# Kernel tuning notes

Hardware: AMD Instinct MI355X
Metric: run time of the kernel (lower is better)

## Reference

```python
import jax, jax.numpy as jnp
import numpy as np

N_NODES = 100000
N_EDGES = 1600000
D = 128
D_FF = 2 * D
BN_EPS = 1e-5


def setup_inputs() -> dict:
    key = jax.random.key(0)
    ks = jax.random.split(key, 16)
    s = lambda k, shp, fan: jax.random.normal(k, shp, jnp.float32) / np.float32(np.sqrt(fan))
    return {
        "x": jax.random.normal(ks[0], (N_NODES, D), jnp.float32),
        "edge_attr": jax.random.normal(ks[1], (N_EDGES, D), jnp.float32),
        "w1g": s(ks[2], (D, D), D),
        "b1g": jnp.zeros((D,), jnp.float32),
        "w2g": s(ks[3], (D, D), D),
        "b2g": jnp.zeros((D,), jnp.float32),
        "bn1_g": jax.random.uniform(ks[4], (D,), jnp.float32, 0.5, 1.5),
        "bn1_b": 0.1 * jax.random.normal(ks[5], (D,), jnp.float32),
        "ff_w1": s(ks[6], (D, D_FF), D),
        "ff_b1": jnp.zeros((D_FF,), jnp.float32),
        "ff_w2": s(ks[7], (D_FF, D), D_FF),
        "ff_b2": jnp.zeros((D,), jnp.float32),
        "bn2_g": jax.random.uniform(ks[8], (D,), jnp.float32, 0.5, 1.5),
        "bn2_b": 0.1 * jax.random.normal(ks[9], (D,), jnp.float32),
        "edge_index": jax.random.randint(ks[10], (2, N_EDGES), 0, N_NODES, jnp.int64 if jax.config.jax_enable_x64 else jnp.int32),
    }


def _batchnorm(h, gamma, beta):
    # training-mode BatchNorm1d: per-batch (node-axis) stats, biased variance
    mean = h.mean(axis=0)
    var = ((h - mean) ** 2).mean(axis=0)
    return gamma * (h - mean) * jax.lax.rsqrt(var + BN_EPS) + beta


def reference(x, edge_attr, w1g, b1g, w2g, b2g, bn1_g, bn1_b,
              ff_w1, ff_b1, ff_w2, ff_b2, bn2_g, bn2_b, edge_index):
    src, dst = edge_index[0], edge_index[1]
    # GINEConv message: relu(x_j + e_ij), scatter-sum into target nodes
    msg = jax.nn.relu(x[src] + edge_attr)                      # [E, D]
    agg = jax.ops.segment_sum(msg, dst, num_segments=N_NODES)  # [N, D]
    h = x + agg                                                # (1+eps)*x with eps=0
    # gin_nn: Linear -> ReLU -> Linear
    h = jax.nn.relu(h @ w1g + b1g) @ w2g + b2g
    h = jax.nn.relu(h)                                         # post-conv relu; dropout=identity (eval)
    h = x + h                                                  # residual
    h = _batchnorm(h, bn1_g, bn1_b)                            # norm1_local
    ff = jax.nn.relu(h @ ff_w1 + ff_b1) @ ff_w2 + ff_b2        # FFN block (dropouts identity)
    h = h + ff
    h = _batchnorm(h, bn2_g, bn2_b)                            # norm2
    return h
```

## Files before the change

### kernel.cpp

```cpp
#include <hip/hip_runtime.h>
#include <hip/hip_bf16.h>

#define NN 100000
#define NE 1600000
#define DD 128
#define DFF 256
#define BN_EPS 1e-5f
#define NND ((size_t)NN * DD)
#define NTILE 6250
#define CAP 64

typedef __attribute__((ext_vector_type(8))) short short8;
typedef __attribute__((ext_vector_type(4))) float f32x4;
typedef __attribute__((ext_vector_type(4))) unsigned short us4;

static __device__ __forceinline__ unsigned short f2bf(float f) {
  union { float f; unsigned u; } v; v.f = f;
  unsigned r = v.u + 0x7fffu + ((v.u >> 16) & 1u);
  return (unsigned short)(r >> 16);
}
static __device__ __forceinline__ float bf2f(unsigned short h) {
  union { unsigned u; float f; } v; v.u = ((unsigned)h) << 16;
  return v.f;
}

__global__ __launch_bounds__(256) void k_prep(const float* __restrict__ x,
    unsigned short* __restrict__ xbf,
    const float* __restrict__ w1g, const float* __restrict__ w2g,
    const float* __restrict__ ffw1, const float* __restrict__ ffw2,
    unsigned short* __restrict__ w1t, unsigned short* __restrict__ w2t,
    unsigned short* __restrict__ fw1t, unsigned short* __restrict__ fw2t) {
  int b = blockIdx.x;
  if (b < 6250) {
    size_t base = ((size_t)b * 256u + threadIdx.x) * 8;
    const f32x4* xp = reinterpret_cast<const f32x4*>(x + base);
    f32x4 a0 = xp[0], a1 = xp[1];
    short8 o;
#pragma unroll
    for (int j = 0; j < 4; ++j) o[j] = (short)f2bf(a0[j]);
#pragma unroll
    for (int j = 0; j < 4; ++j) o[4 + j] = (short)f2bf(a1[j]);
    *reinterpret_cast<short8*>(xbf + base) = o;
  } else {
    int i = (b - 6250) * 256 + threadIdx.x;
    if (i < 16384) { int c = i & 127, k = i >> 7; w1t[c * 128 + k] = f2bf(w1g[k * 128 + c]); }
    else if (i < 32768) { i -= 16384; int c = i & 127, k = i >> 7; w2t[c * 128 + k] = f2bf(w2g[k * 128 + c]); }
    else if (i < 65536) { i -= 32768; int c = i & 255, k = i >> 8; fw1t[c * 128 + k] = f2bf(ffw1[k * 256 + c]); }
    else if (i < 98304) { i -= 65536; int c = i & 127, k = i >> 7; fw2t[c * 256 + k] = f2bf(ffw2[k * 128 + c]); }
  }
}

__global__ __launch_bounds__(256) void k_scatter(const int* __restrict__ ei,
                                                 int* __restrict__ cnt,
                                                 int2* __restrict__ el2) {
  int e = blockIdx.x * 256 + threadIdx.x;
  if (e >= NE) return;
  int s = ei[e], d = ei[NE + e];
  int p = atomicAdd(&cnt[d], 1);
  if (p < CAP) el2[d * CAP + p] = make_int2(e, s);
}

__global__ __launch_bounds__(256) void k_gather(
    const unsigned short* __restrict__ xbf, const float* __restrict__ ea,
    const int* __restrict__ cnt, const int2* __restrict__ el2,
    unsigned short* __restrict__ h0) {
  int n = blockIdx.x * 8 + (threadIdx.x >> 5);
  int q = threadIdx.x & 31;
  int deg = cnt[n];
  deg = deg > CAP ? CAP : deg;
  int beg = n * CAP;
  int end = beg + deg;
  f32x4 acc = (f32x4){0.f, 0.f, 0.f, 0.f};
  int2 E0 = make_int2(0, 0), E1 = E0, E2 = E0, E3 = E0;
  int i = beg;
  if (i     < end) E0 = el2[i];
  if (i + 1 < end) E1 = el2[i + 1];
  if (i + 2 < end) E2 = el2[i + 2];
  if (i + 3 < end) E3 = el2[i + 3];
  for (; i + 4 <= end; i += 4) {
    f32x4 ev0 = *(reinterpret_cast<const f32x4*>(ea + (size_t)E0.x * DD) + q);
    us4  xv0 = *reinterpret_cast<const us4*>(xbf + (size_t)E0.y * DD + q * 4);
    f32x4 ev1 = *(reinterpret_cast<const f32x4*>(ea + (size_t)E1.x * DD) + q);
    us4  xv1 = *reinterpret_cast<const us4*>(xbf + (size_t)E1.y * DD + q * 4);
    f32x4 ev2 = *(reinterpret_cast<const f32x4*>(ea + (size_t)E2.x * DD) + q);
    us4  xv2 = *reinterpret_cast<const us4*>(xbf + (size_t)E2.y * DD + q * 4);
    f32x4 ev3 = *(reinterpret_cast<const f32x4*>(ea + (size_t)E3.x * DD) + q);
    us4  xv3 = *reinterpret_cast<const us4*>(xbf + (size_t)E3.y * DD + q * 4);
    int2 N0 = E0, N1 = E1, N2 = E2, N3 = E3;
    if (i + 4 < end) N0 = el2[i + 4];
    if (i + 5 < end) N1 = el2[i + 5];
    if (i + 6 < end) N2 = el2[i + 6];
    if (i + 7 < end) N3 = el2[i + 7];
#pragma unroll
    for (int c = 0; c < 4; ++c) {
      float m0 = bf2f((unsigned short)xv0[c]) + ev0[c];
      acc[c] += (m0 > 0.f) ? m0 : 0.f;
      float m1 = bf2f((unsigned short)xv1[c]) + ev1[c];
      acc[c] += (m1 > 0.f) ? m1 : 0.f;
      float m2 = bf2f((unsigned short)xv2[c]) + ev2[c];
      acc[c] += (m2 > 0.f) ? m2 : 0.f;
      float m3 = bf2f((unsigned short)xv3[c]) + ev3[c];
      acc[c] += (m3 > 0.f) ? m3 : 0.f;
    }
    E0 = N0; E1 = N1; E2 = N2; E3 = N3;
  }
  if (i < end) {
    f32x4 ev = *(reinterpret_cast<const f32x4*>(ea + (size_t)E0.x * DD) + q);
    us4  xv = *reinterpret_cast<const us4*>(xbf + (size_t)E0.y * DD + q * 4);
#pragma unroll
    for (int c = 0; c < 4; ++c) {
      float m = bf2f((unsigned short)xv[c]) + ev[c];
      acc[c] += (m > 0.f) ? m : 0.f;
    }
  }
  if (i + 1 < end) {
    f32x4 ev = *(reinterpret_cast<const f32x4*>(ea + (size_t)E1.x * DD) + q);
    us4  xv = *reinterpret_cast<const us4*>(xbf + (size_t)E1.y * DD + q * 4);
#pragma unroll
    for (int c = 0; c < 4; ++c) {
      float m = bf2f((unsigned short)xv[c]) + ev[c];
      acc[c] += (m > 0.f) ? m : 0.f;
    }
  }
  if (i + 2 < end) {
    f32x4 ev = *(reinterpret_cast<const f32x4*>(ea + (size_t)E2.x * DD) + q);
    us4  xv = *reinterpret_cast<const us4*>(xbf + (size_t)E2.y * DD + q * 4);
#pragma unroll
    for (int c = 0; c < 4; ++c) {
      float m = bf2f((unsigned short)xv[c]) + ev[c];
      acc[c] += (m > 0.f) ? m : 0.f;
    }
  }
  us4 xs = *reinterpret_cast<const us4*>(xbf + (size_t)n * DD + q * 4);
  union { unsigned short us[4]; unsigned long long u; } pk;
#pragma unroll
  for (int c = 0; c < 4; ++c) pk.us[c] = f2bf(bf2f((unsigned short)xs[c]) + acc[c]);
  *reinterpret_cast<unsigned long long*>(h0 + (size_t)n * DD + q * 4) = pk.u;
}

#define TR1 136
__global__ __launch_bounds__(256) void k_mlp1(const unsigned short* __restrict__ A,
    const unsigned short* __restrict__ W1T, const float* __restrict__ b1,
    const unsigned short* __restrict__ W2T, const float* __restrict__ b2,
    const unsigned short* __restrict__ xbf, float* __restrict__ O,
    float* __restrict__ stats) {
  __shared__ unsigned short tr[4][16 * TR1];
  __shared__ float lds_s[128], lds_q[128];
  if (threadIdx.x < 128) { lds_s[threadIdx.x] = 0.f; lds_q[threadIdx.x] = 0.f; }
  int lane = threadIdx.x & 63, w = threadIdx.x >> 6;
  int tile = blockIdx.x * 4 + w;
  int l15 = lane & 15, g = lane >> 4;
  int row0 = tile * 16;
  __syncthreads();
  if (tile < NTILE) {
    f32x4 acc[8];
#pragma unroll
    for (int ct = 0; ct < 8; ++ct) {
      float b = b1[ct * 16 + l15];
      acc[ct] = (f32x4){b, b, b, b};
    }
    short8 a[4];
#pragma unroll
    for (int kt = 0; kt < 4; ++kt)
      a[kt] = *reinterpret_cast<const short8*>(A + (size_t)(row0 + l15) * DD + kt * 32 + g * 8);
#pragma unroll
    for (int kt = 0; kt < 4; ++kt) {
      int k0 = kt * 32 + g * 8;
#pragma unroll
      for (int ct = 0; ct < 8; ++ct) {
        int c = ct * 16 + l15;
        short8 b = *reinterpret_cast<const short8*>(W1T + (size_t)c * DD + k0);
        acc[ct] = __builtin_amdgcn_mfma_f32_16x16x32_bf16(a[kt], b, acc[ct], 0, 0, 0);
      }
    }
#pragma unroll
    for (int ct = 0; ct < 8; ++ct)
#pragma unroll
      for (int r = 0; r < 4; ++r) {
        float v = acc[ct][r];
        v = v > 0.f ? v : 0.f;
        tr[w][(g * 4 + r) * TR1 + ct * 16 + l15] = f2bf(v);
      }
  }
  __syncthreads();
  if (tile < NTILE) {
    short8 a2[4];
#pragma unroll
    for (int kt = 0; kt < 4; ++kt)
      a2[kt] = *reinterpret_cast<const short8*>(&tr[w][l15 * TR1 + kt * 32 + g * 8]);
    f32x4 acc2[8];
#pragma unroll
    for (int ct = 0; ct < 8; ++ct) {
      float b = b2[ct * 16 + l15];
      acc2[ct] = (f32x4){b, b, b, b};
    }
#pragma unroll
    for (int kt = 0; kt < 4; ++kt) {
      int k0 = kt * 32 + g * 8;
#pragma unroll
      for (int ct = 0; ct < 8; ++ct) {
        int c = ct * 16 + l15;
        short8 b = *reinterpret_cast<const short8*>(W2T + (size_t)c * DD + k0);
        acc2[ct] = __builtin_amdgcn_mfma_f32_16x16x32_bf16(a2[kt], b, acc2[ct], 0, 0, 0);
      }
    }
#pragma unroll
    for (int ct = 0; ct < 8; ++ct) {
      int c = ct * 16 + l15;
      float s = 0.f, q = 0.f;
#pragma unroll
      for (int r = 0; r < 4; ++r) {
        int row = row0 + g * 4 + r;
        float v = acc2[ct][r];
        v = v > 0.f ? v : 0.f;
        v += bf2f(xbf[(size_t)row * DD + c]);
        O[(size_t)row * DD + c] = v;
        s += v; q += v * v;
      }
      s += __shfl_xor(s, 16); s += __shfl_xor(s, 32);
      q += __shfl_xor(q, 16); q += __shfl_xor(q, 32);
      if (g == 0) { atomicAdd(&lds_s[c], s); atomicAdd(&lds_q[c], q); }
    }
  }
  __syncthreads();
  if (threadIdx.x < 128) {
    atomicAdd(&stats[threadIdx.x], lds_s[threadIdx.x]);
    atomicAdd(&stats[128 + threadIdx.x], lds_q[threadIdx.x]);
  }
}

#define TR2 264
__global__ __launch_bounds__(256) void k_mlp2(const float* __restrict__ H,
    const float* __restrict__ stats, const float* __restrict__ bn1g,
    const float* __restrict__ bn1b, const unsigned short* __restrict__ FW1T,
    const float* __restrict__ fb1, const unsigned short* __restrict__ FW2T,
    const float* __restrict__ fb2, float* __restrict__ O, float* __restrict__ stats2) {
  __shared__ unsigned short tr[4][16 * TR2];
  __shared__ float lds_s[128], lds_q[128], ldspar[256];
  int t = threadIdx.x;
  if (t < 128) {
    lds_s[t] = 0.f; lds_q[t] = 0.f;
    float mean = stats[t] * (1.f / NN);
    float var = stats[128 + t] * (1.f / NN) - mean * mean;
    float sc = bn1g[t] * rsqrtf(var + BN_EPS);
    ldspar[t] = sc;
    ldspar[128 + t] = bn1b[t] - mean * sc;
  }
  int lane = t & 63, w = t >> 6;
  int tile = blockIdx.x * 4 + w;
  int l15 = lane & 15, g = lane >> 4;
  int row0 = tile * 16;
  __syncthreads();
  if (tile < NTILE) {
    const float* arow = H + (size_t)(row0 + l15) * DD;
    short8 a1[4];
#pragma unroll
    for (int kt = 0; kt < 4; ++kt) {
      int k0 = kt * 32 + g * 8;
      f32x4 u0 = *reinterpret_cast<const f32x4*>(arow + k0);
      f32x4 u1 = *reinterpret_cast<const f32x4*>(arow + k0 + 4);
      short8 af;
#pragma unroll
      for (int j = 0; j < 4; ++j)
        af[j] = (short)f2bf(ldspar[k0 + j] * u0[j] + ldspar[128 + k0 + j]);
#pragma unroll
      for (int j = 0; j < 4; ++j)
        af[4 + j] = (short)f2bf(ldspar[k0 + 4 + j] * u1[j] + ldspar[128 + k0 + 4 + j]);
      a1[kt] = af;
    }
    f32x4 acc1[16];
#pragma unroll
    for (int ct = 0; ct < 16; ++ct) {
      float b = fb1[ct * 16 + l15];
      acc1[ct] = (f32x4){b, b, b, b};
    }
#pragma unroll
    for (int kt = 0; kt < 4; ++kt) {
      int k0 = kt * 32 + g * 8;
#pragma unroll
      for (int ct = 0; ct < 16; ++ct) {
        int c = ct * 16 + l15;
        short8 b = *reinterpret_cast<const short8*>(FW1T + (size_t)c * DD + k0);
        acc1[ct] = __builtin_amdgcn_mfma_f32_16x16x32_bf16(a1[kt], b, acc1[ct], 0, 0, 0);
      }
    }
#pragma unroll
    for (int ct = 0; ct < 16; ++ct)
#pragma unroll
      for (int r = 0; r < 4; ++r) {
        float v = acc1[ct][r];
        v = v > 0.f ? v : 0.f;
        tr[w][(g * 4 + r) * TR2 + ct * 16 + l15] = f2bf(v);
      }
  }
  __syncthreads();
  if (tile < NTILE) {
    short8 a2[8];
#pragma unroll
    for (int kt = 0; kt < 8; ++kt)
      a2[kt] = *reinterpret_cast<const short8*>(&tr[w][l15 * TR2 + kt * 32 + g * 8]);
    f32x4 acc2[8];
#pragma unroll
    for (int ct = 0; ct < 8; ++ct) {
      float b = fb2[ct * 16 + l15];
      acc2[ct] = (f32x4){b, b, b, b};
    }
#pragma unroll 2
    for (int kt = 0; kt < 8; ++kt) {
      int k0 = kt * 32 + g * 8;
#pragma unroll
      for (int ct = 0; ct < 8; ++ct) {
        int c = ct * 16 + l15;
        short8 b = *reinterpret_cast<const short8*>(FW2T + (size_t)c * DFF + k0);
        acc2[ct] = __builtin_amdgcn_mfma_f32_16x16x32_bf16(a2[kt], b, acc2[ct], 0, 0, 0);
      }
    }
#pragma unroll
    for (int ct = 0; ct < 8; ++ct) {
      int c = ct * 16 + l15;
      float sc = ldspar[c], sh = ldspar[128 + c];
      float s = 0.f, q = 0.f;
#pragma unroll
      for (int r = 0; r < 4; ++r) {
        int row = row0 + g * 4 + r;
        float h1v = sc * O[(size_t)row * DD + c] + sh;
        float v = acc2[ct][r] + h1v;
        O[(size_t)row * DD + c] = v;
        s += v; q += v * v;
      }
      s += __shfl_xor(s, 16); s += __shfl_xor(s, 32);
      q += __shfl_xor(q, 16); q += __shfl_xor(q, 32);
      if (g == 0) { atomicAdd(&lds_s[c], s); atomicAdd(&lds_q[c], q); }
    }
  }
  __syncthreads();
  if (t < 128) {
    atomicAdd(&stats2[t], lds_s[t]);
    atomicAdd(&stats2[128 + t], lds_q[t]);
  }
}

__global__ __launch_bounds__(256) void k_bnfinal(float* __restrict__ h,
    const float* __restrict__ st, const float* __restrict__ gm,
    const float* __restrict__ bt) {
  size_t base = ((size_t)blockIdx.x * 256u + threadIdx.x) * 4;
  int c0 = (int)(base & 127);
  f32x4 v = *reinterpret_cast<f32x4*>(h + base);
#pragma unroll
  for (int j = 0; j < 4; ++j) {
    int c = c0 + j;
    float mean = st[c] * (1.f / NN);
    float var = st[128 + c] * (1.f / NN) - mean * mean;
    float sc = gm[c] * rsqrtf(var + BN_EPS);
    float sh = bt[c] - mean * sc;
    v[j] = sc * v[j] + sh;
  }
  *reinterpret_cast<f32x4*>(h + base) = v;
}

extern "C" void kernel_launch(void* const* d_in, const int* in_sizes, int n_in,
                              void* d_out, int out_size, void* d_ws, size_t ws_size,
                              hipStream_t stream) {
  const float* x    = (const float*)d_in[0];
  const float* ea   = (const float*)d_in[1];
  const float* w1g  = (const float*)d_in[2];
  const float* b1g  = (const float*)d_in[3];
  const float* w2g  = (const float*)d_in[4];
  const float* b2g  = (const float*)d_in[5];
  const float* bn1g = (const float*)d_in[6];
  const float* bn1b = (const float*)d_in[7];
  const float* ffw1 = (const float*)d_in[8];
  const float* ffb1 = (const float*)d_in[9];
  const float* ffw2 = (const float*)d_in[10];
  const float* ffb2 = (const float*)d_in[11];
  const float* bn2g = (const float*)d_in[12];
  const float* bn2b = (const float*)d_in[13];
  const int*   eidx = (const int*)d_in[14];
  float* out = (float*)d_out;

  char* ws = (char*)d_ws;
  int2* el2    = (int2*)(ws);
  int*  cnt    = (int*)(ws + 51200000);
  float* stats = (float*)(ws + 51600000);
  unsigned short* w1t  = (unsigned short*)(ws + 51602048);
  unsigned short* w2t  = (unsigned short*)(ws + 51634816);
  unsigned short* fw1t = (unsigned short*)(ws + 51667584);
  unsigned short* fw2t = (unsigned short*)(ws + 51733120);
  unsigned short* xbf  = (unsigned short*)(ws + 51798656);
  unsigned short* hbf  = (unsigned short*)(ws + 77398656);

  hipMemsetAsync(cnt, 0, 402048, stream);

  k_prep<<<6634, 256, 0, stream>>>(x, xbf, w1g, w2g, ffw1, ffw2,
                                   w1t, w2t, fw1t, fw2t);

  k_scatter<<<6250, 256, 0, stream>>>(eidx, cnt, el2);

  k_gather<<<12500, 256, 0, stream>>>(xbf, ea, cnt, el2, hbf);

  k_mlp1<<<1563, 256, 0, stream>>>(hbf, w1t, b1g, w2t, b2g, xbf, out, stats);
  k_mlp2<<<1563, 256, 0, stream>>>(out, stats, bn1g, bn1b,
                                   fw1t, ffb1, fw2t, ffb2, out, stats + 256);
  k_bnfinal<<<12500, 256, 0, stream>>>(out, stats + 256, bn2g, bn2b);
}
```

Before: 633.4 us.

## Fuse prep with edge scatter, add nontemporal hints, drop block syncs in MLP kernels

Merges the bf16 conversion/weight-transpose kernel and the edge-bucketing scatter kernel into one launch, and writes the packed edge entries with nontemporal stores. The gather now reads edge attributes with nontemporal loads so this single-use stream is kept from evicting the reused x rows. In both MLP kernels the block-wide __syncthreads between the two GEMM stages is removed, since each wave only touches its own LDS slice. mlp2 also keeps the bf16 normalized residual in LDS instead of re-reading it from global memory and re-normalizing, which trades residual precision (bf16 rather than fp32) for less memory traffic.

```diff
diff --git a/kernel.cpp b/kernel.cpp
--- a/kernel.cpp
+++ b/kernel.cpp
@@ -24,12 +24,14 @@
   return v.f;
 }
 
-__global__ __launch_bounds__(256) void k_prep(const float* __restrict__ x,
+__global__ __launch_bounds__(256) void k_prepscat(const float* __restrict__ x,
     unsigned short* __restrict__ xbf,
     const float* __restrict__ w1g, const float* __restrict__ w2g,
     const float* __restrict__ ffw1, const float* __restrict__ ffw2,
     unsigned short* __restrict__ w1t, unsigned short* __restrict__ w2t,
-    unsigned short* __restrict__ fw1t, unsigned short* __restrict__ fw2t) {
+    unsigned short* __restrict__ fw1t, unsigned short* __restrict__ fw2t,
+    const int* __restrict__ ei, int* __restrict__ cnt,
+    long long* __restrict__ el2) {
   int b = blockIdx.x;
   if (b < 6250) {
     size_t base = ((size_t)b * 256u + threadIdx.x) * 8;
@@ -41,23 +43,24 @@
 #pragma unroll
     for (int j = 0; j < 4; ++j) o[4 + j] = (short)f2bf(a1[j]);
     *reinterpret_cast<short8*>(xbf + base) = o;
-  } else {
+  } else if (b < 6634) {
     int i = (b - 6250) * 256 + threadIdx.x;
     if (i < 16384) { int c = i & 127, k = i >> 7; w1t[c * 128 + k] = f2bf(w1g[k * 128 + c]); }
     else if (i < 32768) { i -= 16384; int c = i & 127, k = i >> 7; w2t[c * 128 + k] = f2bf(w2g[k * 128 + c]); }
     else if (i < 65536) { i -= 32768; int c = i & 255, k = i >> 8; fw1t[c * 128 + k] = f2bf(ffw1[k * 256 + c]); }
     else if (i < 98304) { i -= 65536; int c = i & 127, k = i >> 7; fw2t[c * 256 + k] = f2bf(ffw2[k * 128 + c]); }
-  }
-}
-
-__global__ __launch_bounds__(256) void k_scatter(const int* __restrict__ ei,
-                                                 int* __restrict__ cnt,
-                                                 int2* __restrict__ el2) {
-  int e = blockIdx.x * 256 + threadIdx.x;
-  if (e >= NE) return;
-  int s = ei[e], d = ei[NE + e];
-  int p = atomicAdd(&cnt[d], 1);
-  if (p < CAP) el2[d * CAP + p] = make_int2(e, s);
+  } else {
+    int e = (b - 6634) * 256 + threadIdx.x;
+    if (e < NE) {
+      int s = ei[e], d = ei[NE + e];
+      int p = atomicAdd(&cnt[d], 1);
+      if (p < CAP) {
+        long long pk = (long long)((unsigned long long)(unsigned)e |
+                                   ((unsigned long long)(unsigned)s << 32));
+        __builtin_nontemporal_store(pk, &el2[d * CAP + p]);
+      }
+    }
+  }
 }
 
 __global__ __launch_bounds__(256) void k_gather(
@@ -78,13 +81,13 @@
   if (i + 2 < end) E2 = el2[i + 2];
   if (i + 3 < end) E3 = el2[i + 3];
   for (; i + 4 <= end; i += 4) {
-    f32x4 ev0 = *(reinterpret_cast<const f32x4*>(ea + (size_t)E0.x * DD) + q);
+    f32x4 ev0 = __builtin_nontemporal_load(reinterpret_cast<const f32x4*>(ea + (size_t)E0.x * DD) + q);
     us4  xv0 = *reinterpret_cast<const us4*>(xbf + (size_t)E0.y * DD + q * 4);
-    f32x4 ev1 = *(reinterpret_cast<const f32x4*>(ea + (size_t)E1.x * DD) + q);
+    f32x4 ev1 = __builtin_nontemporal_load(reinterpret_cast<const f32x4*>(ea + (size_t)E1.x * DD) + q);
     us4  xv1 = *reinterpret_cast<const us4*>(xbf + (size_t)E1.y * DD + q * 4);
-    f32x4 ev2 = *(reinterpret_cast<const f32x4*>(ea + (size_t)E2.x * DD) + q);
+    f32x4 ev2 = __builtin_nontemporal_load(reinterpret_cast<const f32x4*>(ea + (size_t)E2.x * DD) + q);
     us4  xv2 = *reinterpret_cast<const us4*>(xbf + (size_t)E2.y * DD + q * 4);
-    f32x4 ev3 = *(reinterpret_cast<const f32x4*>(ea + (size_t)E3.x * DD) + q);
+    f32x4 ev3 = __builtin_nontemporal_load(reinterpret_cast<const f32x4*>(ea + (size_t)E3.x * DD) + q);
     us4  xv3 = *reinterpret_cast<const us4*>(xbf + (size_t)E3.y * DD + q * 4);
     int2 N0 = E0, N1 = E1, N2 = E2, N3 = E3;
     if (i + 4 < end) N0 = el2[i + 4];
@@ -105,7 +108,7 @@
     E0 = N0; E1 = N1; E2 = N2; E3 = N3;
   }
   if (i < end) {
-    f32x4 ev = *(reinterpret_cast<const f32x4*>(ea + (size_t)E0.x * DD) + q);
+    f32x4 ev = __builtin_nontemporal_load(reinterpret_cast<const f32x4*>(ea + (size_t)E0.x * DD) + q);
     us4  xv = *reinterpret_cast<const us4*>(xbf + (size_t)E0.y * DD + q * 4);
 #pragma unroll
     for (int c = 0; c < 4; ++c) {
@@ -114,7 +117,7 @@
     }
   }
   if (i + 1 < end) {
-    f32x4 ev = *(reinterpret_cast<const f32x4*>(ea + (size_t)E1.x * DD) + q);
+    f32x4 ev = __builtin_nontemporal_load(reinterpret_cast<const f32x4*>(ea + (size_t)E1.x * DD) + q);
     us4  xv = *reinterpret_cast<const us4*>(xbf + (size_t)E1.y * DD + q * 4);
 #pragma unroll
     for (int c = 0; c < 4; ++c) {
@@ -123,7 +126,7 @@
     }
   }
   if (i + 2 < end) {
-    f32x4 ev = *(reinterpret_cast<const f32x4*>(ea + (size_t)E2.x * DD) + q);
+    f32x4 ev = __builtin_nontemporal_load(reinterpret_cast<const f32x4*>(ea + (size_t)E2.x * DD) + q);
     us4  xv = *reinterpret_cast<const us4*>(xbf + (size_t)E2.y * DD + q * 4);
 #pragma unroll
     for (int c = 0; c < 4; ++c) {
@@ -181,9 +184,6 @@
         v = v > 0.f ? v : 0.f;
         tr[w][(g * 4 + r) * TR1 + ct * 16 + l15] = f2bf(v);
       }
-  }
-  __syncthreads();
-  if (tile < NTILE) {
     short8 a2[4];
 #pragma unroll
     for (int kt = 0; kt < 4; ++kt)
@@ -236,6 +236,7 @@
     const float* __restrict__ fb1, const unsigned short* __restrict__ FW2T,
     const float* __restrict__ fb2, float* __restrict__ O, float* __restrict__ stats2) {
   __shared__ unsigned short tr[4][16 * TR2];
+  __shared__ unsigned short resid[4][16 * DD];
   __shared__ float lds_s[128], lds_q[128], ldspar[256];
   int t = threadIdx.x;
   if (t < 128) {
@@ -267,6 +268,7 @@
       for (int j = 0; j < 4; ++j)
         af[4 + j] = (short)f2bf(ldspar[k0 + 4 + j] * u1[j] + ldspar[128 + k0 + 4 + j]);
       a1[kt] = af;
+      *reinterpret_cast<short8*>(&resid[w][l15 * DD + k0]) = af;
     }
     f32x4 acc1[16];
 #pragma unroll
@@ -292,9 +294,6 @@
         v = v > 0.f ? v : 0.f;
         tr[w][(g * 4 + r) * TR2 + ct * 16 + l15] = f2bf(v);
       }
-  }
-  __syncthreads();
-  if (tile < NTILE) {
     short8 a2[8];
 #pragma unroll
     for (int kt = 0; kt < 8; ++kt)
@@ -318,12 +317,11 @@
 #pragma unroll
     for (int ct = 0; ct < 8; ++ct) {
       int c = ct * 16 + l15;
-      float sc = ldspar[c], sh = ldspar[128 + c];
       float s = 0.f, q = 0.f;
 #pragma unroll
       for (int r = 0; r < 4; ++r) {
         int row = row0 + g * 4 + r;
-        float h1v = sc * O[(size_t)row * DD + c] + sh;
+        float h1v = bf2f(resid[w][(g * 4 + r) * DD + c]);
         float v = acc2[ct][r] + h1v;
         O[(size_t)row * DD + c] = v;
         s += v; q += v * v;
@@ -379,6 +377,7 @@
   float* out = (float*)d_out;
 
   char* ws = (char*)d_ws;
+  long long* el2ll = (long long*)(ws);
   int2* el2    = (int2*)(ws);
   int*  cnt    = (int*)(ws + 51200000);
   float* stats = (float*)(ws + 51600000);
@@ -391,10 +390,8 @@
 
   hipMemsetAsync(cnt, 0, 402048, stream);
 
-  k_prep<<<6634, 256, 0, stream>>>(x, xbf, w1g, w2g, ffw1, ffw2,
-                                   w1t, w2t, fw1t, fw2t);
-
-  k_scatter<<<6250, 256, 0, stream>>>(eidx, cnt, el2);
+  k_prepscat<<<12884, 256, 0, stream>>>(x, xbf, w1g, w2g, ffw1, ffw2,
+                                        w1t, w2t, fw1t, fw2t, eidx, cnt, el2ll);
 
   k_gather<<<12500, 256, 0, stream>>>(xbf, ea, cnt, el2, hbf);
 
```

New measurement: 647.2 us. 1.02x slower.

## Stage edge lists in LDS, double-buffer gather loads, drop per-warp MLP barriers

Applied to the files above, without the earlier changes.

The gather kernel now has each 32-lane group copy its node's edge list into shared memory, padding it to a multiple of four. It then processes edges with two register buffers of four gathered rows each, so loads for the next chunk are issued while the current chunk is accumulated. This is meant to hide the latency of the dependent index-then-row loads. Both MLP kernels also drop the block-wide __syncthreads between writing and reading each warp's private transpose buffer. That relies on each warp only touching its own tr[w] slice, which risks a missing intra-wave ordering fence.

```diff
diff --git a/kernel.cpp b/kernel.cpp
--- a/kernel.cpp
+++ b/kernel.cpp
@@ -60,75 +60,64 @@
   if (p < CAP) el2[d * CAP + p] = make_int2(e, s);
 }
 
+#define GLOAD(ev, xv, base)                                                    \
+  do {                                                                         \
+    _Pragma("unroll")                                                          \
+    for (int j = 0; j < 4; ++j) {                                              \
+      int2 E = sidx[g][(base) + j];                                            \
+      ev[j] = *(reinterpret_cast<const f32x4*>(ea + (size_t)E.x * DD) + q);    \
+      xv[j] = *reinterpret_cast<const us4*>(xbf + (size_t)E.y * DD + q * 4);   \
+    }                                                                          \
+  } while (0)
+
+#define GCONS(ev, xv, cval)                                                    \
+  do {                                                                         \
+    _Pragma("unroll")                                                          \
+    for (int j = 0; j < 4; ++j) {                                              \
+      if (j < (cval)) {                                                        \
+        _Pragma("unroll")                                                      \
+        for (int c = 0; c < 4; ++c) {                                          \
+          float m = bf2f((unsigned short)xv[j][c]) + ev[j][c];                 \
+          acc[c] += (m > 0.f) ? m : 0.f;                                       \
+        }                                                                      \
+      }                                                                        \
+    }                                                                          \
+  } while (0)
+
 __global__ __launch_bounds__(256) void k_gather(
     const unsigned short* __restrict__ xbf, const float* __restrict__ ea,
     const int* __restrict__ cnt, const int2* __restrict__ el2,
     unsigned short* __restrict__ h0) {
-  int n = blockIdx.x * 8 + (threadIdx.x >> 5);
+  __shared__ int2 sidx[8][CAP];
+  int g = threadIdx.x >> 5;
+  int n = blockIdx.x * 8 + g;
   int q = threadIdx.x & 31;
   int deg = cnt[n];
   deg = deg > CAP ? CAP : deg;
+  int pad4 = (deg + 3) & ~3;
   int beg = n * CAP;
-  int end = beg + deg;
+  if (q < deg) sidx[g][q] = el2[beg + q];
+  else if (q < pad4) sidx[g][q] = make_int2(0, 0);
+  int q2 = q + 32;
+  if (q2 < deg) sidx[g][q2] = el2[beg + q2];
+  else if (q2 < pad4) sidx[g][q2] = make_int2(0, 0);
+
   f32x4 acc = (f32x4){0.f, 0.f, 0.f, 0.f};
-  int2 E0 = make_int2(0, 0), E1 = E0, E2 = E0, E3 = E0;
-  int i = beg;
-  if (i     < end) E0 = el2[i];
-  if (i + 1 < end) E1 = el2[i + 1];
-  if (i + 2 < end) E2 = el2[i + 2];
-  if (i + 3 < end) E3 = el2[i + 3];
-  for (; i + 4 <= end; i += 4) {
-    f32x4 ev0 = *(reinterpret_cast<const f32x4*>(ea + (size_t)E0.x * DD) + q);
-    us4  xv0 = *reinterpret_cast<const us4*>(xbf + (size_t)E0.y * DD + q * 4);
-    f32x4 ev1 = *(reinterpret_cast<const f32x4*>(ea + (size_t)E1.x * DD) + q);
-    us4  xv1 = *reinterpret_cast<const us4*>(xbf + (size_t)E1.y * DD + q * 4);
-    f32x4 ev2 = *(reinterpret_cast<const f32x4*>(ea + (size_t)E2.x * DD) + q);
-    us4  xv2 = *reinterpret_cast<const us4*>(xbf + (size_t)E2.y * DD + q * 4);
-    f32x4 ev3 = *(reinterpret_cast<const f32x4*>(ea + (size_t)E3.x * DD) + q);
-    us4  xv3 = *reinterpret_cast<const us4*>(xbf + (size_t)E3.y * DD + q * 4);
-    int2 N0 = E0, N1 = E1, N2 = E2, N3 = E3;
-    if (i + 4 < end) N0 = el2[i + 4];
-    if (i + 5 < end) N1 = el2[i + 5];
-    if (i + 6 < end) N2 = el2[i + 6];
-    if (i + 7 < end) N3 = el2[i + 7];
-#pragma unroll
-    for (int c = 0; c < 4; ++c) {
-      float m0 = bf2f((unsigned short)xv0[c]) + ev0[c];
-      acc[c] += (m0 > 0.f) ? m0 : 0.f;
-      float m1 = bf2f((unsigned short)xv1[c]) + ev1[c];
-      acc[c] += (m1 > 0.f) ? m1 : 0.f;
-      float m2 = bf2f((unsigned short)xv2[c]) + ev2[c];
-      acc[c] += (m2 > 0.f) ? m2 : 0.f;
-      float m3 = bf2f((unsigned short)xv3[c]) + ev3[c];
-      acc[c] += (m3 > 0.f) ? m3 : 0.f;
-    }
-    E0 = N0; E1 = N1; E2 = N2; E3 = N3;
-  }
-  if (i < end) {
-    f32x4 ev = *(reinterpret_cast<const f32x4*>(ea + (size_t)E0.x * DD) + q);
-    us4  xv = *reinterpret_cast<const us4*>(xbf + (size_t)E0.y * DD + q * 4);
-#pragma unroll
-    for (int c = 0; c < 4; ++c) {
-      float m = bf2f((unsigned short)xv[c]) + ev[c];
-      acc[c] += (m > 0.f) ? m : 0.f;
-    }
-  }
-  if (i + 1 < end) {
-    f32x4 ev = *(reinterpret_cast<const f32x4*>(ea + (size_t)E1.x * DD) + q);
-    us4  xv = *reinterpret_cast<const us4*>(xbf + (size_t)E1.y * DD + q * 4);
-#pragma unroll
-    for (int c = 0; c < 4; ++c) {
-      float m = bf2f((unsigned short)xv[c]) + ev[c];
-      acc[c] += (m > 0.f) ? m : 0.f;
-    }
-  }
-  if (i + 2 < end) {
-    f32x4 ev = *(reinterpret_cast<const f32x4*>(ea + (size_t)E2.x * DD) + q);
-    us4  xv = *reinterpret_cast<const us4*>(xbf + (size_t)E2.y * DD + q * 4);
-#pragma unroll
-    for (int c = 0; c < 4; ++c) {
-      float m = bf2f((unsigned short)xv[c]) + ev[c];
-      acc[c] += (m > 0.f) ? m : 0.f;
+  int nch = (deg + 3) >> 2;
+  f32x4 evA[4], evB[4];
+  us4 xvA[4], xvB[4];
+  if (nch > 0) {
+    GLOAD(evA, xvA, 0);
+    if (nch > 1) GLOAD(evB, xvB, 4);
+    for (int c = 0; c < nch; c += 2) {
+      int cA = deg - c * 4; cA = cA > 4 ? 4 : cA;
+      GCONS(evA, xvA, cA);
+      if (c + 2 < nch) GLOAD(evA, xvA, (c + 2) * 4);
+      if (c + 1 < nch) {
+        int cB = deg - (c + 1) * 4; cB = cB > 4 ? 4 : cB;
+        GCONS(evB, xvB, cB);
+        if (c + 3 < nch) GLOAD(evB, xvB, (c + 3) * 4);
+      }
     }
   }
   us4 xs = *reinterpret_cast<const us4*>(xbf + (size_t)n * DD + q * 4);
@@ -181,9 +170,6 @@
         v = v > 0.f ? v : 0.f;
         tr[w][(g * 4 + r) * TR1 + ct * 16 + l15] = f2bf(v);
       }
-  }
-  __syncthreads();
-  if (tile < NTILE) {
     short8 a2[4];
 #pragma unroll
     for (int kt = 0; kt < 4; ++kt)
@@ -292,9 +278,6 @@
         v = v > 0.f ? v : 0.f;
         tr[w][(g * 4 + r) * TR2 + ct * 16 + l15] = f2bf(v);
       }
-  }
-  __syncthreads();
-  if (tile < NTILE) {
     short8 a2[8];
 #pragma unroll
     for (int kt = 0; kt < 8; ++kt)
```

Measured after the change: 625.3 us. No clear change (-1.3%).
